# Performance work log

Measured on AMD Instinct MI355X. Metric: run time of the kernel, lower is better.

The kernel has to match this reference:

```python
import jax, jax.numpy as jnp
import numpy as np

DIM = 512
PDIM = 64
NUM_HEAD = 8
HEAD_DIM = DIM // NUM_HEAD
SCALE = HEAD_DIM ** -0.5
EPS = 1e-6


def setup_inputs() -> dict:
    key = jax.random.key(0)
    ks = jax.random.split(key, 8)
    B, N = 8, 2048
    x_token = jax.random.normal(ks[0], (B, N, DIM), dtype=jnp.float32)
    x_path = jax.random.normal(ks[1], (B, N, PDIM), dtype=jnp.float32)
    idx_cluster = jax.random.randint(ks[2], (B, N), 0, 16, dtype=jnp.int32)
    # weights stored as [in, out] (y = x @ W + b), matching torch Linear math
    Wqk = jax.random.normal(ks[3], (DIM, 2 * DIM), dtype=jnp.float32) * 0.02
    Wv = jax.random.normal(ks[4], (DIM, DIM), dtype=jnp.float32) * 0.02
    Wpv = jax.random.normal(ks[5], (PDIM, PDIM), dtype=jnp.float32) * 0.02
    Wproj = jax.random.normal(ks[6], (DIM, DIM), dtype=jnp.float32) * 0.02
    bproj = jax.random.normal(ks[7], (DIM,), dtype=jnp.float32) * 0.02
    return {"x_token": x_token, "x_path": x_path, "idx_cluster": idx_cluster,
            "cluster_num": 16, "Wqk": Wqk, "Wv": Wv, "Wpv": Wpv,
            "Wproj": Wproj, "bproj": bproj}


def reference(x_token, x_path, idx_cluster, cluster_num, Wqk, Wv, Wpv, Wproj, bproj):
    B, N, C = x_token.shape
    qk = x_token @ Wqk                      # [B,N,2C]
    q, k = qk[..., :C], qk[..., C:]
    v = x_token @ Wv                        # [B,N,C]
    pv = x_path @ Wpv                       # dead code in original; kept for fidelity

    idx_shuffle = jnp.argsort(idx_cluster, axis=1)          # [B,N]
    idx_restore = jnp.argsort(idx_shuffle, axis=1)

    v_s = jnp.take_along_axis(v, idx_shuffle[..., None], axis=1)
    pv_s = jnp.take_along_axis(pv, idx_shuffle[..., None], axis=1)  # unused (faithful)

    attn_map = jnp.einsum('bic,bjc->bij', q, k) * SCALE     # [B,N,N]

    # torch does two gathers, both with dim=1; the second index is constant along
    # rows, so attn2[b,i,j] = attn_map[b, idx_shuffle[b, idx_shuffle[b,j]], j]
    double = jnp.take_along_axis(idx_shuffle, idx_shuffle, axis=1)  # [B,N]
    col_vals = jnp.take_along_axis(jnp.swapaxes(attn_map, 1, 2), double[..., None], axis=2)[..., 0]  # [B,N]
    attn = jnp.broadcast_to(col_vals[:, None, :], (B, N, N))

    # contiguous per-cluster block mask in sorted order == equality of sorted ids
    s = jnp.sort(idx_cluster, axis=1)
    mask = (s[:, :, None] == s[:, None, :]) & (s[:, :, None] < cluster_num)

    attn = jnp.where(mask, attn, jnp.float32(-1e9))
    attn = jnp.exp(attn.astype(jnp.float32))
    attn = (attn + EPS / N) / (jnp.sum(attn, axis=-1, keepdims=True) + EPS)

    out = attn @ v_s                                         # [B,N,C]
    out = jnp.swapaxes(out, 1, 2).reshape(B, N, C)           # faithful layout scramble
    out = jnp.take_along_axis(out, idx_restore[..., None], axis=1)
    x_out = out @ Wproj + bproj
    return x_out, attn_map
```

## Files before the change

kernel.cpp:

```cpp
#include <hip/hip_runtime.h>
#include <hip/hip_bf16.h>

typedef __attribute__((ext_vector_type(8))) short short8;
typedef __attribute__((ext_vector_type(4))) float floatx4;

__device__ __forceinline__ unsigned short f2bfu(float f) {
    unsigned u = __float_as_uint(f);
    unsigned rounding = 0x7fffu + ((u >> 16) & 1u);
    return (unsigned short)((u + rounding) >> 16);
}
__device__ __forceinline__ float bfu2f(unsigned short u) {
    return __uint_as_float(((unsigned)u) << 16);
}

__device__ __forceinline__ void async_ld16(const void* g, void* l) {
    __builtin_amdgcn_global_load_lds(
        (const __attribute__((address_space(1))) void*)g,
        (__attribute__((address_space(3))) void*)l, 16, 0, 0);
}

#define B_  8
#define N_  2048
#define C_  512
#define NC_ 16

__global__ __launch_bounds__(256) void cvt_x(const float4* __restrict__ x,
                                             unsigned short* __restrict__ xbf) {
    size_t i = (size_t)blockIdx.x * 256 + threadIdx.x;
    float4 f = x[i];
    unsigned short u0 = f2bfu(f.x), u1 = f2bfu(f.y), u2 = f2bfu(f.z), u3 = f2bfu(f.w);
    uint2 p;
    p.x = (unsigned)u0 | ((unsigned)u1 << 16);
    p.y = (unsigned)u2 | ((unsigned)u3 << 16);
    *(uint2*)(xbf + 4 * i) = p;
}

__global__ __launch_bounds__(256) void cvt_wqkv(const float* __restrict__ Wqk,
                                                const float* __restrict__ Wv,
                                                unsigned short* __restrict__ WT) {
    int id = blockIdx.x * 256 + threadIdx.x;
    int n = id >> 9, k = id & 511;
    float v = (n < 1024) ? Wqk[(size_t)k * 1024 + n] : Wv[(size_t)k * 512 + (n - 1024)];
    WT[id] = f2bfu(v);
}

__global__ __launch_bounds__(256) void cvt_wproj(const float* __restrict__ W,
                                                 unsigned short* __restrict__ WT) {
    int id = blockIdx.x * 256 + threadIdx.x;
    int n = id >> 9, k = id & 511;
    WT[id] = f2bfu(W[(size_t)k * 512 + n]);
}

__global__ __launch_bounds__(256) void sort_kernel(const int* __restrict__ idx_cluster,
                                                   int* __restrict__ shuf,
                                                   int* __restrict__ restore,
                                                   int* __restrict__ svals,
                                                   int* __restrict__ dbl,
                                                   int* __restrict__ cstart) {
    int b = blockIdx.x, t = threadIdx.x;
    __shared__ int vals[N_];
    __shared__ int seghist[256 * 17];
    __shared__ int cbase[NC_], ctot[NC_];
    __shared__ int shufs[N_];
    const int* src = idx_cluster + (size_t)b * N_;
    for (int j = t; j < N_; j += 256) vals[j] = src[j];
    for (int c = 0; c < NC_; ++c) seghist[t * 17 + c] = 0;
    __syncthreads();
    for (int i = 0; i < 8; ++i) {
        int c = vals[t * 8 + i];
        seghist[t * 17 + c]++;
    }
    __syncthreads();
    if (t < NC_) {
        int run = 0;
        for (int s = 0; s < 256; ++s) {
            int x = seghist[s * 17 + t];
            seghist[s * 17 + t] = run;
            run += x;
        }
        ctot[t] = run;
    }
    __syncthreads();
    if (t == 0) {
        int run = 0;
        for (int c = 0; c < NC_; ++c) {
            cbase[c] = run;
            cstart[b * 17 + c] = run;
            run += ctot[c];
        }
        cstart[b * 17 + NC_] = run;
    }
    __syncthreads();
    for (int i = 0; i < 8; ++i) {
        int p = t * 8 + i;
        int c = vals[p];
        int pos = cbase[c] + seghist[t * 17 + c];
        seghist[t * 17 + c]++;
        shufs[pos] = p;
    }
    __syncthreads();
    for (int j = t; j < N_; j += 256) {
        int sj = shufs[j];
        shuf[(size_t)b * N_ + j] = sj;
        svals[(size_t)b * N_ + j] = vals[sj];
        restore[(size_t)b * N_ + sj] = j;
        dbl[(size_t)b * N_ + j] = shufs[sj];
    }
}

template <int MODE>
__global__ __launch_bounds__(256) void gemm_bt(const unsigned short* __restrict__ A,
                                               const unsigned short* __restrict__ Bt,
                                               float* __restrict__ outF,
                                               unsigned short* __restrict__ outQ,
                                               unsigned short* __restrict__ outK,
                                               unsigned short* __restrict__ outV,
                                               const float* __restrict__ bias) {
    constexpr int K = 512;
    int t = threadIdx.x;
    int lane = t & 63, wave = t >> 6;
    int wm = (wave & 1) * 64, wn = (wave >> 1) * 64;
    int m0 = blockIdx.y * 128, n0 = blockIdx.x * 128;
    if (MODE == 1) {
        size_t b = blockIdx.z;
        A += b * (size_t)N_ * 512;
        Bt += b * (size_t)N_ * 512;
        outF += b * (size_t)N_ * N_;
    }
    __shared__ __align__(16) unsigned short As[128 * 64];
    __shared__ __align__(16) unsigned short Bs[128 * 64];
    floatx4 acc[4][4] = {};
    int l15 = lane & 15, q4 = lane >> 4;
    int srow = lane >> 3, schk = lane & 7;
    int sgc = schk ^ srow;
    int xr = l15 & 7;

    for (int k0 = 0; k0 < K; k0 += 64) {
        __syncthreads();
#pragma unroll
        for (int i = 0; i < 4; ++i) {
            int cid = i * 4 + wave;
            int row = cid * 8 + srow;
            async_ld16(A + (size_t)(m0 + row) * 512 + k0 + sgc * 8, (char*)As + cid * 1024);
            async_ld16(Bt + (size_t)(n0 + row) * 512 + k0 + sgc * 8, (char*)Bs + cid * 1024);
        }
        __syncthreads();
#pragma unroll
        for (int kk = 0; kk < 2; ++kk) {
            int csw = (((kk * 4 + q4) ^ xr) * 8);
            short8 af[4], bfr[4];
#pragma unroll
            for (int mi = 0; mi < 4; ++mi)
                af[mi] = *(const short8*)(&As[(wm + mi * 16 + l15) * 64 + csw]);
#pragma unroll
            for (int ni = 0; ni < 4; ++ni)
                bfr[ni] = *(const short8*)(&Bs[(wn + ni * 16 + l15) * 64 + csw]);
#pragma unroll
            for (int mi = 0; mi < 4; ++mi)
#pragma unroll
                for (int ni = 0; ni < 4; ++ni)
                    acc[mi][ni] = __builtin_amdgcn_mfma_f32_16x16x32_bf16(af[mi], bfr[ni], acc[mi][ni], 0, 0, 0);
        }
    }
#pragma unroll
    for (int mi = 0; mi < 4; ++mi) {
#pragma unroll
        for (int ni = 0; ni < 4; ++ni) {
#pragma unroll
            for (int r = 0; r < 4; ++r) {
                int row = m0 + wm + mi * 16 + q4 * 4 + r;
                int col = n0 + wn + ni * 16 + l15;
                float v = acc[mi][ni][r];
                if (MODE == 0) {
                    unsigned short u = f2bfu(v);
                    if (col < 512)       outQ[(size_t)row * 512 + col] = u;
                    else if (col < 1024) outK[(size_t)row * 512 + col - 512] = u;
                    else                 outV[(size_t)row * 512 + col - 1024] = u;
                } else if (MODE == 1) {
                    outF[(size_t)row * N_ + col] = v * 0.125f;
                } else {
                    outF[(size_t)row * 512 + col] = v + bias[col];
                }
            }
        }
    }
}

__global__ __launch_bounds__(256) void cluster_reduce(const float* __restrict__ attn,
                                                      const int* __restrict__ shuf,
                                                      const int* __restrict__ dbl,
                                                      const int* __restrict__ cstart,
                                                      const unsigned short* __restrict__ vbf,
                                                      float* __restrict__ Ot) {
    int c = blockIdx.x, b = blockIdx.y, t = threadIdx.x;
    int start = cstart[b * 17 + c], end = cstart[b * 17 + c + 1];
    int n = end - start;
    if (n <= 0) return;
    __shared__ float e_lds[N_];
    __shared__ float Sred;
    if (t == 0) Sred = 0.f;
    __syncthreads();
    float ps = 0.f;
    for (int i = t; i < n; i += 256) {
        int j = start + i;
        int dj = dbl[(size_t)b * N_ + j];
        float cv = attn[(size_t)b * N_ * N_ + (size_t)dj * N_ + j];
        float e = expf(cv);
        e_lds[i] = e;
        ps += e;
    }
    atomicAdd(&Sred, ps);
    __syncthreads();
    float t0 = 0.f, t1 = 0.f;
    for (int i = 0; i < n; ++i) {
        float e = e_lds[i];
        int row = shuf[(size_t)b * N_ + start + i];
        const unsigned short* vr = vbf + ((size_t)b * N_ + row) * 512;
        t0 += e * bfu2f(vr[t]);
        t1 += e * bfu2f(vr[t + 256]);
    }
    float inv = 1.f / Sred;
    Ot[((size_t)b * 512 + t) * 16 + c] = t0 * inv;
    Ot[((size_t)b * 512 + t + 256) * 16 + c] = t1 * inv;
}

__global__ __launch_bounds__(256) void build_out3(const float* __restrict__ Ot,
                                                  const int* __restrict__ svals,
                                                  const int* __restrict__ restore,
                                                  unsigned int* __restrict__ out3u) {
    int rg = blockIdx.x, b = blockIdx.y, t = threadIdx.x;
    __shared__ float Olds[512 * 16];
    __shared__ int slds[N_];
    for (int i = t; i < 512 * 16; i += 256) Olds[i] = Ot[(size_t)b * 512 * 16 + i];
    for (int i = t; i < N_; i += 256) slds[i] = svals[(size_t)b * N_ + i];
    __syncthreads();
    for (int n = rg * 64; n < rg * 64 + 64; ++n) {
        int r = restore[(size_t)b * N_ + n];
        int rq = r >> 2;
        int bj = (r & 3) * 512;
        int c0 = slds[bj + 2 * t];
        int c1 = slds[bj + 2 * t + 1];
        float v0 = Olds[rq * 16 + c0];
        float v1 = Olds[rq * 16 + c1];
        unsigned p = (unsigned)f2bfu(v0) | ((unsigned)f2bfu(v1) << 16);
        out3u[((size_t)b * N_ + n) * 256 + t] = p;
    }
}

extern "C" void kernel_launch(void* const* d_in, const int* in_sizes, int n_in,
                              void* d_out, int out_size, void* d_ws, size_t ws_size,
                              hipStream_t stream) {
    const float* x_token = (const float*)d_in[0];
    const int* idx_cluster = (const int*)d_in[2];
    const float* Wqk = (const float*)d_in[4];
    const float* Wv = (const float*)d_in[5];
    const float* Wproj = (const float*)d_in[7];
    const float* bproj = (const float*)d_in[8];

    float* x_out = (float*)d_out;
    float* attn = x_out + (size_t)B_ * N_ * C_;

    char* ws = (char*)d_ws;
    size_t off = 0;
    auto alloc = [&](size_t bytes) {
        void* p = ws + off;
        off += (bytes + 255) & ~(size_t)255;
        return p;
    };
    unsigned short* WqkvT = (unsigned short*)alloc(1536 * 512 * 2);
    unsigned short* WprojT = (unsigned short*)alloc(512 * 512 * 2);
    unsigned short* xbf = (unsigned short*)alloc((size_t)B_ * N_ * C_ * 2);
    unsigned short* qbf = (unsigned short*)alloc((size_t)B_ * N_ * C_ * 2);
    unsigned short* kbf = (unsigned short*)alloc((size_t)B_ * N_ * C_ * 2);
    unsigned short* vbf = (unsigned short*)alloc((size_t)B_ * N_ * C_ * 2);
    int* shuf = (int*)alloc((size_t)B_ * N_ * 4);
    int* restore = (int*)alloc((size_t)B_ * N_ * 4);
    int* svals = (int*)alloc((size_t)B_ * N_ * 4);
    int* dbl = (int*)alloc((size_t)B_ * N_ * 4);
    int* cstart = (int*)alloc(B_ * 17 * 4);
    float* Ot = (float*)alloc((size_t)B_ * 512 * 16 * 4);

    cvt_x<<<dim3((B_ * N_ * C_) / (256 * 4)), dim3(256), 0, stream>>>((const float4*)x_token, xbf);
    cvt_wqkv<<<dim3((1536 * 512) / 256), dim3(256), 0, stream>>>(Wqk, Wv, WqkvT);
    cvt_wproj<<<dim3((512 * 512) / 256), dim3(256), 0, stream>>>(Wproj, WprojT);

    sort_kernel<<<dim3(B_), dim3(256), 0, stream>>>(idx_cluster, shuf, restore, svals, dbl, cstart);

    gemm_bt<0><<<dim3(1536 / 128, 16384 / 128, 1), dim3(256), 0, stream>>>(
        xbf, WqkvT, nullptr, qbf, kbf, vbf, nullptr);

    gemm_bt<1><<<dim3(N_ / 128, N_ / 128, B_), dim3(256), 0, stream>>>(
        qbf, kbf, attn, nullptr, nullptr, nullptr, nullptr);

    cluster_reduce<<<dim3(NC_, B_), dim3(256), 0, stream>>>(attn, shuf, dbl, cstart, vbf, Ot);

    build_out3<<<dim3(N_ / 64, B_), dim3(256), 0, stream>>>(Ot, svals, restore, (unsigned int*)xbf);

    gemm_bt<2><<<dim3(512 / 128, 16384 / 128, 1), dim3(256), 0, stream>>>(
        xbf, WprojT, x_out, nullptr, nullptr, nullptr, bproj);
}
```

Measured before the change: 346.6 us.

## Enlarge GEMM tiles to 256x128 and vectorize cluster reduce and output build

The GEMM block tile grows from 128x128 to 256x128, so each wave computes a 64x128 strip with 32 accumulators. This raises data reuse per LDS load and halves the grid, at the cost of more registers and larger LDS use. cluster_reduce now splits rows across the four waves, loads 16-byte vectors of V, reduces the exp sum with shuffles, and sums partials through LDS. build_out3 gives each wave its own rows and writes 16-byte stores.

```diff
diff --git a/kernel.cpp b/kernel.cpp
--- a/kernel.cpp
+++ b/kernel.cpp
@@ -109,27 +109,27 @@
 }
 
 template <int MODE>
-__global__ __launch_bounds__(256) void gemm_bt(const unsigned short* __restrict__ A,
-                                               const unsigned short* __restrict__ Bt,
-                                               float* __restrict__ outF,
-                                               unsigned short* __restrict__ outQ,
-                                               unsigned short* __restrict__ outK,
-                                               unsigned short* __restrict__ outV,
-                                               const float* __restrict__ bias) {
+__global__ __launch_bounds__(256, 2) void gemm_bt(const unsigned short* __restrict__ A,
+                                                  const unsigned short* __restrict__ Bt,
+                                                  float* __restrict__ outF,
+                                                  unsigned short* __restrict__ outQ,
+                                                  unsigned short* __restrict__ outK,
+                                                  unsigned short* __restrict__ outV,
+                                                  const float* __restrict__ bias) {
     constexpr int K = 512;
     int t = threadIdx.x;
     int lane = t & 63, wave = t >> 6;
-    int wm = (wave & 1) * 64, wn = (wave >> 1) * 64;
-    int m0 = blockIdx.y * 128, n0 = blockIdx.x * 128;
+    int wm = wave * 64;
+    int m0 = blockIdx.y * 256, n0 = blockIdx.x * 128;
     if (MODE == 1) {
         size_t b = blockIdx.z;
         A += b * (size_t)N_ * 512;
         Bt += b * (size_t)N_ * 512;
         outF += b * (size_t)N_ * N_;
     }
-    __shared__ __align__(16) unsigned short As[128 * 64];
+    __shared__ __align__(16) unsigned short As[256 * 64];
     __shared__ __align__(16) unsigned short Bs[128 * 64];
-    floatx4 acc[4][4] = {};
+    floatx4 acc[4][8] = {};
     int l15 = lane & 15, q4 = lane >> 4;
     int srow = lane >> 3, schk = lane & 7;
     int sgc = schk ^ srow;
@@ -138,38 +138,43 @@
     for (int k0 = 0; k0 < K; k0 += 64) {
         __syncthreads();
 #pragma unroll
+        for (int i = 0; i < 8; ++i) {
+            int cid = i * 4 + wave;
+            int row = cid * 8 + srow;
+            async_ld16(A + (size_t)(m0 + row) * 512 + k0 + sgc * 8, (char*)As + cid * 1024);
+        }
+#pragma unroll
         for (int i = 0; i < 4; ++i) {
             int cid = i * 4 + wave;
             int row = cid * 8 + srow;
-            async_ld16(A + (size_t)(m0 + row) * 512 + k0 + sgc * 8, (char*)As + cid * 1024);
             async_ld16(Bt + (size_t)(n0 + row) * 512 + k0 + sgc * 8, (char*)Bs + cid * 1024);
         }
         __syncthreads();
 #pragma unroll
         for (int kk = 0; kk < 2; ++kk) {
             int csw = (((kk * 4 + q4) ^ xr) * 8);
-            short8 af[4], bfr[4];
+            short8 af[4], bfr[8];
 #pragma unroll
             for (int mi = 0; mi < 4; ++mi)
                 af[mi] = *(const short8*)(&As[(wm + mi * 16 + l15) * 64 + csw]);
 #pragma unroll
-            for (int ni = 0; ni < 4; ++ni)
-                bfr[ni] = *(const short8*)(&Bs[(wn + ni * 16 + l15) * 64 + csw]);
+            for (int ni = 0; ni < 8; ++ni)
+                bfr[ni] = *(const short8*)(&Bs[(ni * 16 + l15) * 64 + csw]);
 #pragma unroll
             for (int mi = 0; mi < 4; ++mi)
 #pragma unroll
-                for (int ni = 0; ni < 4; ++ni)
+                for (int ni = 0; ni < 8; ++ni)
                     acc[mi][ni] = __builtin_amdgcn_mfma_f32_16x16x32_bf16(af[mi], bfr[ni], acc[mi][ni], 0, 0, 0);
         }
     }
 #pragma unroll
     for (int mi = 0; mi < 4; ++mi) {
 #pragma unroll
-        for (int ni = 0; ni < 4; ++ni) {
+        for (int ni = 0; ni < 8; ++ni) {
 #pragma unroll
             for (int r = 0; r < 4; ++r) {
                 int row = m0 + wm + mi * 16 + q4 * 4 + r;
-                int col = n0 + wn + ni * 16 + l15;
+                int col = n0 + ni * 16 + l15;
                 float v = acc[mi][ni][r];
                 if (MODE == 0) {
                     unsigned short u = f2bfu(v);
@@ -193,10 +198,12 @@
                                                       const unsigned short* __restrict__ vbf,
                                                       float* __restrict__ Ot) {
     int c = blockIdx.x, b = blockIdx.y, t = threadIdx.x;
+    int lane = t & 63, w = t >> 6;
     int start = cstart[b * 17 + c], end = cstart[b * 17 + c + 1];
     int n = end - start;
     if (n <= 0) return;
     __shared__ float e_lds[N_];
+    __shared__ float part[4 * 512];
     __shared__ float Sred;
     if (t == 0) Sred = 0.f;
     __syncthreads();
@@ -204,24 +211,31 @@
     for (int i = t; i < n; i += 256) {
         int j = start + i;
         int dj = dbl[(size_t)b * N_ + j];
-        float cv = attn[(size_t)b * N_ * N_ + (size_t)dj * N_ + j];
-        float e = expf(cv);
+        float e = expf(attn[(size_t)b * N_ * N_ + (size_t)dj * N_ + j]);
         e_lds[i] = e;
         ps += e;
     }
-    atomicAdd(&Sred, ps);
-    __syncthreads();
-    float t0 = 0.f, t1 = 0.f;
-    for (int i = 0; i < n; ++i) {
+#pragma unroll
+    for (int off = 32; off; off >>= 1) ps += __shfl_down(ps, off);
+    if (lane == 0) atomicAdd(&Sred, ps);
+    __syncthreads();
+    float acc[8] = {};
+    for (int i = w; i < n; i += 4) {
         float e = e_lds[i];
         int row = shuf[(size_t)b * N_ + start + i];
-        const unsigned short* vr = vbf + ((size_t)b * N_ + row) * 512;
-        t0 += e * bfu2f(vr[t]);
-        t1 += e * bfu2f(vr[t + 256]);
-    }
+        short8 vv = *(const short8*)(vbf + ((size_t)b * N_ + row) * 512 + lane * 8);
+#pragma unroll
+        for (int u = 0; u < 8; ++u) acc[u] += e * bfu2f((unsigned short)vv[u]);
+    }
+#pragma unroll
+    for (int u = 0; u < 8; ++u) part[w * 512 + lane * 8 + u] = acc[u];
+    __syncthreads();
     float inv = 1.f / Sred;
-    Ot[((size_t)b * 512 + t) * 16 + c] = t0 * inv;
-    Ot[((size_t)b * 512 + t + 256) * 16 + c] = t1 * inv;
+    int d0 = t, d1 = t + 256;
+    float s0 = part[d0] + part[512 + d0] + part[1024 + d0] + part[1536 + d0];
+    float s1 = part[d1] + part[512 + d1] + part[1024 + d1] + part[1536 + d1];
+    Ot[((size_t)b * 512 + d0) * 16 + c] = s0 * inv;
+    Ot[((size_t)b * 512 + d1) * 16 + c] = s1 * inv;
 }
 
 __global__ __launch_bounds__(256) void build_out3(const float* __restrict__ Ot,
@@ -229,21 +243,26 @@
                                                   const int* __restrict__ restore,
                                                   unsigned int* __restrict__ out3u) {
     int rg = blockIdx.x, b = blockIdx.y, t = threadIdx.x;
+    int lane = t & 63, w = t >> 6;
     __shared__ float Olds[512 * 16];
     __shared__ int slds[N_];
     for (int i = t; i < 512 * 16; i += 256) Olds[i] = Ot[(size_t)b * 512 * 16 + i];
     for (int i = t; i < N_; i += 256) slds[i] = svals[(size_t)b * N_ + i];
     __syncthreads();
-    for (int n = rg * 64; n < rg * 64 + 64; ++n) {
+    for (int k = 0; k < 16; ++k) {
+        int n = rg * 64 + w * 16 + k;
         int r = restore[(size_t)b * N_ + n];
         int rq = r >> 2;
         int bj = (r & 3) * 512;
-        int c0 = slds[bj + 2 * t];
-        int c1 = slds[bj + 2 * t + 1];
-        float v0 = Olds[rq * 16 + c0];
-        float v1 = Olds[rq * 16 + c1];
-        unsigned p = (unsigned)f2bfu(v0) | ((unsigned)f2bfu(v1) << 16);
-        out3u[((size_t)b * N_ + n) * 256 + t] = p;
+        int4 cA = *(const int4*)(&slds[bj + lane * 8]);
+        int4 cB = *(const int4*)(&slds[bj + lane * 8 + 4]);
+        const float* Or = &Olds[rq * 16];
+        uint4 p;
+        p.x = (unsigned)f2bfu(Or[cA.x]) | ((unsigned)f2bfu(Or[cA.y]) << 16);
+        p.y = (unsigned)f2bfu(Or[cA.z]) | ((unsigned)f2bfu(Or[cA.w]) << 16);
+        p.z = (unsigned)f2bfu(Or[cB.x]) | ((unsigned)f2bfu(Or[cB.y]) << 16);
+        p.w = (unsigned)f2bfu(Or[cB.z]) | ((unsigned)f2bfu(Or[cB.w]) << 16);
+        *(uint4*)(&out3u[((size_t)b * N_ + n) * 256 + lane * 4]) = p;
     }
 }
 
@@ -286,16 +305,16 @@
 
     sort_kernel<<<dim3(B_), dim3(256), 0, stream>>>(idx_cluster, shuf, restore, svals, dbl, cstart);
 
-    gemm_bt<0><<<dim3(1536 / 128, 16384 / 128, 1), dim3(256), 0, stream>>>(
+    gemm_bt<0><<<dim3(1536 / 128, 16384 / 256, 1), dim3(256), 0, stream>>>(
         xbf, WqkvT, nullptr, qbf, kbf, vbf, nullptr);
 
-    gemm_bt<1><<<dim3(N_ / 128, N_ / 128, B_), dim3(256), 0, stream>>>(
+    gemm_bt<1><<<dim3(N_ / 128, N_ / 256, B_), dim3(256), 0, stream>>>(
         qbf, kbf, attn, nullptr, nullptr, nullptr, nullptr);
 
     cluster_reduce<<<dim3(NC_, B_), dim3(256), 0, stream>>>(attn, shuf, dbl, cstart, vbf, Ot);
 
     build_out3<<<dim3(N_ / 64, B_), dim3(256), 0, stream>>>(Ot, svals, restore, (unsigned int*)xbf);
 
-    gemm_bt<2><<<dim3(512 / 128, 16384 / 128, 1), dim3(256), 0, stream>>>(
+    gemm_bt<2><<<dim3(512 / 128, 16384 / 256, 1), dim3(256), 0, stream>>>(
         xbf, WprojT, x_out, nullptr, nullptr, nullptr, bproj);
 }
```

Measured after the change: 372.5 us. 1.07x slower.
